# Optimization experiments

Measured on AMD Instinct MI355X. Metric: run time of the kernel, lower is better.

Reference implementation:

```python
import jax, jax.numpy as jnp
import numpy as np

H = 8
LN_EPS = 1e-5

def setup_inputs() -> dict:
    key = jax.random.key(0)
    k1, k2, k3, k4 = jax.random.split(key, 4)
    bh, q_len, dk = 64, 1024, 64
    return {
        "query": jax.random.normal(k1, (bh, q_len, dk), dtype=jnp.float32),
        "key": jax.random.normal(k2, (bh, q_len, dk), dtype=jnp.float32),
        "value": jax.random.normal(k3, (bh, q_len, dk), dtype=jnp.float32),
        "head_att": jax.random.normal(k4, (H, H), dtype=jnp.float32),
        "ln_w": jnp.ones((H,), dtype=jnp.float32),
        "ln_b": jnp.zeros((H,), dtype=jnp.float32),
    }

def reference(query, key, value, head_att, ln_w, ln_b):
    bh, q_len, dk = query.shape
    k_len = key.shape[1]
    # scores: (bh, q, k)
    scores = jnp.einsum("bqd,bkd->bqk", query, key) / jnp.sqrt(jnp.asarray(dk, query.dtype))
    attn = jax.nn.softmax(scores, axis=-1)
    # view as (B, H, q, k) then move heads last: (B, q, k, H)
    a = attn.reshape(-1, H, q_len, k_len).transpose(0, 2, 3, 1)
    # DeepViT re-attention: cross-head mixing matmul
    a = a @ head_att  # (B, q, k, H)
    # LayerNorm over head dim
    mu = a.mean(axis=-1, keepdims=True)
    var = ((a - mu) ** 2).mean(axis=-1, keepdims=True)
    a = (a - mu) * jax.lax.rsqrt(var + LN_EPS) * ln_w + ln_b
    # back to (B, H, q, k)
    a = a.transpose(0, 3, 1, 2)
    att_map = a.mean(axis=1)  # (B, q, k)
    attention = a.reshape(bh, q_len, k_len)
    out = jnp.einsum("bqk,bkd->bqd", attention, value)
    return (out, att_map)
```

## Files before the change

kernel.cpp:

```cpp
#include <hip/hip_runtime.h>
#include <hip/hip_bf16.h>

typedef _Float16 f16;
typedef f16 f16x8 __attribute__((ext_vector_type(8)));
typedef f16 f16x4 __attribute__((ext_vector_type(4)));
typedef float f32x4 __attribute__((ext_vector_type(4)));

#define QL 1024
#define KL 1024
#define DKD 64
#define NH 8
#define LNEPS 1e-5f

__global__ __launch_bounds__(256) void prep_cvt(const float* __restrict__ src,
                                                f16* __restrict__ dst, float scale) {
  int i = (blockIdx.x * 256 + threadIdx.x) * 4;
  float4 v = *reinterpret_cast<const float4*>(src + i);
  f16x4 o;
  o[0] = (f16)(v.x * scale); o[1] = (f16)(v.y * scale);
  o[2] = (f16)(v.z * scale); o[3] = (f16)(v.w * scale);
  *reinterpret_cast<f16x4*>(dst + i) = o;
}

__global__ __launch_bounds__(256) void prep_vt(const float* __restrict__ V, f16* __restrict__ vt) {
  __shared__ float t[32][33];
  const int bh = blockIdx.z, k0 = blockIdx.x * 32, d0 = blockIdx.y * 32;
  const float* src = V + ((size_t)bh * KL + k0) * DKD + d0;
#pragma unroll
  for (int j = 0; j < 4; ++j) {
    int kk = threadIdx.y * 4 + j;
    t[kk][threadIdx.x] = src[kk * DKD + threadIdx.x];
  }
  __syncthreads();
  f16* dst = vt + ((size_t)bh * DKD + d0) * KL + k0;
#pragma unroll
  for (int j = 0; j < 4; ++j) {
    int dd = threadIdx.y * 4 + j;
    dst[dd * KL + threadIdx.x] = (f16)t[threadIdx.x][dd];
  }
}

__global__ __launch_bounds__(256) void stats_kernel(const f16* __restrict__ qf,
    const f16* __restrict__ kf, float* __restrict__ rowsum) {
  const int tid = threadIdx.x;
  const int lane = tid & 63, w = tid >> 6;
  const int m = lane & 15, g = lane >> 4;
  const int id = blockIdx.x;
  const int bh = (id & 7) * 8 + ((id >> 3) & 7);
  const int q0 = (id >> 6) * 64 + w * 16;

  f16x8 qv[2];
#pragma unroll
  for (int dc = 0; dc < 2; ++dc)
    qv[dc] = *reinterpret_cast<const f16x8*>(
        qf + ((size_t)bh * QL + q0 + m) * DKD + dc * 32 + g * 8);

  float part[4] = {0.f, 0.f, 0.f, 0.f};
#pragma unroll 2
  for (int kt = 0; kt < 64; ++kt) {
    const f16* kb = kf + ((size_t)bh * KL + kt * 16 + m) * DKD + g * 8;
    f16x8 k0f = *reinterpret_cast<const f16x8*>(kb);
    f16x8 k1f = *reinterpret_cast<const f16x8*>(kb + 32);
    f32x4 acc = {0.f, 0.f, 0.f, 0.f};
    acc = __builtin_amdgcn_mfma_f32_16x16x32_f16(qv[0], k0f, acc, 0, 0, 0);
    acc = __builtin_amdgcn_mfma_f32_16x16x32_f16(qv[1], k1f, acc, 0, 0, 0);
#pragma unroll
    for (int ri = 0; ri < 4; ++ri) part[ri] += __expf(acc[ri]);
  }
#pragma unroll
  for (int ri = 0; ri < 4; ++ri) {
    float v = part[ri];
    v += __shfl_xor(v, 1); v += __shfl_xor(v, 2);
    v += __shfl_xor(v, 4); v += __shfl_xor(v, 8);
    part[ri] = v;
  }
  if (m == 0) {
#pragma unroll
    for (int ri = 0; ri < 4; ++ri) rowsum[(size_t)bh * QL + q0 + g * 4 + ri] = part[ri];
  }
}

__global__ __launch_bounds__(256) void main_kernel(
    const f16* __restrict__ qf, const f16* __restrict__ kf, const f16* __restrict__ vt,
    const float* __restrict__ rowsum,
    const float* __restrict__ hA, const float* __restrict__ lnw, const float* __restrict__ lnb,
    float* __restrict__ outp, float* __restrict__ part1, float* __restrict__ att_map) {
  __shared__ __align__(16) f16 y_lds[2][NH][16][64];

  const int tid = threadIdx.x;
  const int lane = tid & 63, w = tid >> 6;
  const int m = lane & 15, g = lane >> 4;
  const int id = blockIdx.x;
  const int b = id & 7, kc = (id >> 3) & 1, q0 = (id >> 4) * 16;

  float haR[64], wR[8], bR[8];
#pragma unroll
  for (int j = 0; j < 64; ++j) haR[j] = hA[j];
#pragma unroll
  for (int j = 0; j < 8; ++j) { wR[j] = lnw[j]; bR[j] = lnb[j]; }

  f16x8 qv[NH][2];
#pragma unroll
  for (int h = 0; h < NH; ++h)
#pragma unroll
    for (int dc = 0; dc < 2; ++dc)
      qv[h][dc] = *reinterpret_cast<const f16x8*>(
          qf + (((size_t)(b * NH + h)) * QL + q0 + m) * DKD + dc * 32 + g * 8);

  float inv_rs[NH][4];
#pragma unroll
  for (int h = 0; h < NH; ++h)
#pragma unroll
    for (int ri = 0; ri < 4; ++ri)
      inv_rs[h][ri] = 1.0f / rowsum[(size_t)(b * NH + h) * QL + q0 + g * 4 + ri];

  const size_t kbase_b = (size_t)b * NH * KL;
  f32x4 oacc[2][4];
#pragma unroll
  for (int hp = 0; hp < 2; ++hp)
#pragma unroll
    for (int dt = 0; dt < 4; ++dt) oacc[hp][dt] = (f32x4){0.f, 0.f, 0.f, 0.f};

  for (int kt = 0; kt < 8; ++kt) {
    const int kbase = kc * 512 + kt * 64;
    const int kcol = kbase + w * 16;
    const int buf = kt & 1;

    f32x4 pacc[NH];
    {
      const f16* kb = kf + (kbase_b + kcol + m) * DKD + g * 8;
#pragma unroll
      for (int h = 0; h < NH; ++h) {
        f16x8 k0f = *reinterpret_cast<const f16x8*>(kb + (size_t)h * KL * DKD);
        f16x8 k1f = *reinterpret_cast<const f16x8*>(kb + (size_t)h * KL * DKD + 32);
        f32x4 acc = {0.f, 0.f, 0.f, 0.f};
        acc = __builtin_amdgcn_mfma_f32_16x16x32_f16(qv[h][0], k0f, acc, 0, 0, 0);
        acc = __builtin_amdgcn_mfma_f32_16x16x32_f16(qv[h][1], k1f, acc, 0, 0, 0);
        pacc[h] = acc;
      }
    }
#pragma unroll
    for (int h = 0; h < NH; ++h)
#pragma unroll
      for (int ri = 0; ri < 4; ++ri)
        pacc[h][ri] = __expf(pacc[h][ri]) * inv_rs[h][ri];

#pragma unroll
    for (int ri = 0; ri < 4; ++ri) {
      const int qq = g * 4 + ri;
      float mixed[8];
      float mu = 0.f;
#pragma unroll
      for (int hh = 0; hh < 8; ++hh) {
        float s = 0.f;
#pragma unroll
        for (int j = 0; j < 8; ++j) s = fmaf(pacc[j][ri], haR[j * 8 + hh], s);
        mixed[hh] = s; mu += s;
      }
      mu *= 0.125f;
      float var = 0.f;
#pragma unroll
      for (int hh = 0; hh < 8; ++hh) { float d = mixed[hh] - mu; var = fmaf(d, d, var); }
      var *= 0.125f;
      const float rsv = rsqrtf(var + LNEPS);
      float am = 0.f;
      const int kidx = ((((2 * w + (m >> 3)) ^ (qq & 7)) << 3) | (m & 7));
#pragma unroll
      for (int hh = 0; hh < 8; ++hh) {
        float y = (mixed[hh] - mu) * rsv * wR[hh] + bR[hh];
        am += y;
        y_lds[buf][hh][qq][kidx] = (f16)y;
      }
      att_map[((size_t)b * QL + q0 + qq) * KL + kcol + m] = am * 0.125f;
    }
    __syncthreads();

#pragma unroll
    for (int hp = 0; hp < 2; ++hp) {
      const int hh = w + hp * 4;
      const f16* vb = vt + (((size_t)(b * NH + hh)) * DKD + m) * KL + kbase + g * 8;
#pragma unroll
      for (int ks = 0; ks < 2; ++ks) {
        const f16x8 af = *reinterpret_cast<const f16x8*>(
            &y_lds[buf][hh][m][((ks * 4 + g) ^ (m & 7)) << 3]);
#pragma unroll
        for (int dt = 0; dt < 4; ++dt) {
          f16x8 vf = *reinterpret_cast<const f16x8*>(vb + (size_t)dt * 16 * KL + ks * 32);
          oacc[hp][dt] = __builtin_amdgcn_mfma_f32_16x16x32_f16(af, vf, oacc[hp][dt], 0, 0, 0);
        }
      }
    }
  }

  float* dst = kc ? part1 : outp;
#pragma unroll
  for (int hp = 0; hp < 2; ++hp) {
    const int hh = w + hp * 4;
#pragma unroll
    for (int dt = 0; dt < 4; ++dt)
#pragma unroll
      for (int ri = 0; ri < 4; ++ri)
        dst[(((size_t)(b * NH + hh)) * QL + q0 + g * 4 + ri) * DKD + dt * 16 + m] =
            oacc[hp][dt][ri];
  }
}

__global__ __launch_bounds__(256) void reduce_kernel(const float* __restrict__ p1,
                                                     float* __restrict__ outp) {
  size_t i = ((size_t)blockIdx.x * 256 + threadIdx.x) * 4;
  float4 a = *reinterpret_cast<const float4*>(outp + i);
  float4 c = *reinterpret_cast<const float4*>(p1 + i);
  a.x += c.x; a.y += c.y; a.z += c.z; a.w += c.w;
  *reinterpret_cast<float4*>(outp + i) = a;
}

extern "C" void kernel_launch(void* const* d_in, const int* in_sizes, int n_in,
                              void* d_out, int out_size, void* d_ws, size_t ws_size,
                              hipStream_t stream) {
  const float* Qm  = (const float*)d_in[0];
  const float* Km  = (const float*)d_in[1];
  const float* Vm  = (const float*)d_in[2];
  const float* hA  = (const float*)d_in[3];
  const float* lnw = (const float*)d_in[4];
  const float* lnb = (const float*)d_in[5];
  float* outp = (float*)d_out;
  float* att_map = outp + (size_t)64 * QL * DKD;

  char* ws = (char*)d_ws;
  f16* kfp   = (f16*)ws;
  f16* vtp   = (f16*)(ws + (size_t)8388608);
  f16* qfp   = (f16*)(ws + (size_t)16777216);
  float* rsm = (float*)(ws + (size_t)25165824);
  float* p1  = (float*)(ws + (size_t)25427968);

  prep_cvt<<<4096, 256, 0, stream>>>(Km, kfp, 1.0f);
  prep_cvt<<<4096, 256, 0, stream>>>(Qm, qfp, 0.125f);
  prep_vt<<<dim3(32, 2, 64), dim3(32, 8), 0, stream>>>(Vm, vtp);
  stats_kernel<<<1024, 256, 0, stream>>>(qfp, kfp, rsm);
  main_kernel<<<1024, 256, 0, stream>>>(qfp, kfp, vtp, rsm, hA, lnw, lnb, outp, p1, att_map);
  reduce_kernel<<<4096, 256, 0, stream>>>(p1, outp);
}
```

Baseline: 240.8 us.

## Split fused attention into mix and PV kernels with packed fp16 head mixing

```diff
diff --git a/kernel.cpp b/kernel.cpp
--- a/kernel.cpp
+++ b/kernel.cpp
@@ -1,10 +1,12 @@
 #include <hip/hip_runtime.h>
-#include <hip/hip_bf16.h>
 
 typedef _Float16 f16;
 typedef f16 f16x8 __attribute__((ext_vector_type(8)));
 typedef f16 f16x4 __attribute__((ext_vector_type(4)));
+typedef f16 hf2 __attribute__((ext_vector_type(2)));
 typedef float f32x4 __attribute__((ext_vector_type(4)));
+typedef unsigned int u32;
+typedef unsigned short u16;
 
 #define QL 1024
 #define KL 1024
@@ -12,9 +14,27 @@
 #define NH 8
 #define LNEPS 1e-5f
 
-__global__ __launch_bounds__(256) void prep_cvt(const float* __restrict__ src,
-                                                f16* __restrict__ dst, float scale) {
-  int i = (blockIdx.x * 256 + threadIdx.x) * 4;
+__device__ __forceinline__ hf2 pkrtz(float a, float b) {
+  return __builtin_bit_cast(hf2, __builtin_amdgcn_cvt_pkrtz(a, b));
+}
+__device__ __forceinline__ hf2 bch(u32 v) { return __builtin_bit_cast(hf2, v); }
+
+__global__ __launch_bounds__(256) void prep_qk(const float* __restrict__ K,
+    const float* __restrict__ Q, f16* __restrict__ kf, f16* __restrict__ qf,
+    const float* __restrict__ hA, const float* __restrict__ lnw,
+    const float* __restrict__ lnb, u32* __restrict__ prm) {
+  const int bid = blockIdx.x;
+  if (bid == 0 && threadIdx.x < 80) {
+    int t = threadIdx.x;
+    float v = t < 64 ? hA[t] : (t < 72 ? lnw[t - 64] : lnb[t - 72]);
+    u16 hb = __builtin_bit_cast(u16, (f16)v);
+    prm[t] = (u32)hb * 0x10001u;
+  }
+  const bool isQ = bid >= 4096;
+  const float* src = isQ ? Q : K;
+  f16* dst = isQ ? qf : kf;
+  const float scale = isQ ? 0.125f : 1.0f;
+  int i = ((bid & 4095) * 256 + threadIdx.x) * 4;
   float4 v = *reinterpret_cast<const float4*>(src + i);
   f16x4 o;
   o[0] = (f16)(v.x * scale); o[1] = (f16)(v.y * scale);
@@ -40,30 +60,30 @@
   }
 }
 
-__global__ __launch_bounds__(256) void stats_kernel(const f16* __restrict__ qf,
-    const f16* __restrict__ kf, float* __restrict__ rowsum) {
-  const int tid = threadIdx.x;
-  const int lane = tid & 63, w = tid >> 6;
+__global__ __launch_bounds__(256) void stats4(const f16* __restrict__ qf,
+    const f16* __restrict__ kf, float* __restrict__ prs4) {
+  const int tid = threadIdx.x, lane = tid & 63, w = tid >> 6;
   const int m = lane & 15, g = lane >> 4;
-  const int id = blockIdx.x;
-  const int bh = (id & 7) * 8 + ((id >> 3) & 7);
-  const int q0 = (id >> 6) * 64 + w * 16;
-
-  f16x8 qv[2];
-#pragma unroll
-  for (int dc = 0; dc < 2; ++dc)
-    qv[dc] = *reinterpret_cast<const f16x8*>(
-        qf + ((size_t)bh * QL + q0 + m) * DKD + dc * 32 + g * 8);
+  int id = blockIdx.x;
+  const int b = id & 7; id >>= 3;
+  const int h = id & 7; id >>= 3;
+  const int kq = id & 3; const int q64 = id >> 2;
+  const int bh = b * 8 + h;
+  const int q0 = q64 * 64 + w * 16;
+
+  const f16* qp = qf + ((size_t)bh * QL + q0 + m) * DKD + g * 8;
+  f16x8 qv0 = *reinterpret_cast<const f16x8*>(qp);
+  f16x8 qv1 = *reinterpret_cast<const f16x8*>(qp + 32);
 
   float part[4] = {0.f, 0.f, 0.f, 0.f};
 #pragma unroll 2
-  for (int kt = 0; kt < 64; ++kt) {
-    const f16* kb = kf + ((size_t)bh * KL + kt * 16 + m) * DKD + g * 8;
+  for (int kt = 0; kt < 16; ++kt) {
+    const f16* kb = kf + ((size_t)bh * KL + kq * 256 + kt * 16 + m) * DKD + g * 8;
     f16x8 k0f = *reinterpret_cast<const f16x8*>(kb);
     f16x8 k1f = *reinterpret_cast<const f16x8*>(kb + 32);
     f32x4 acc = {0.f, 0.f, 0.f, 0.f};
-    acc = __builtin_amdgcn_mfma_f32_16x16x32_f16(qv[0], k0f, acc, 0, 0, 0);
-    acc = __builtin_amdgcn_mfma_f32_16x16x32_f16(qv[1], k1f, acc, 0, 0, 0);
+    acc = __builtin_amdgcn_mfma_f32_16x16x32_f16(qv0, k0f, acc, 0, 0, 0);
+    acc = __builtin_amdgcn_mfma_f32_16x16x32_f16(qv1, k1f, acc, 0, 0, 0);
 #pragma unroll
     for (int ri = 0; ri < 4; ++ri) part[ri] += __expf(acc[ri]);
   }
@@ -76,142 +96,146 @@
   }
   if (m == 0) {
 #pragma unroll
-    for (int ri = 0; ri < 4; ++ri) rowsum[(size_t)bh * QL + q0 + g * 4 + ri] = part[ri];
-  }
-}
-
-__global__ __launch_bounds__(256) void main_kernel(
-    const f16* __restrict__ qf, const f16* __restrict__ kf, const f16* __restrict__ vt,
-    const float* __restrict__ rowsum,
-    const float* __restrict__ hA, const float* __restrict__ lnw, const float* __restrict__ lnb,
-    float* __restrict__ outp, float* __restrict__ part1, float* __restrict__ att_map) {
-  __shared__ __align__(16) f16 y_lds[2][NH][16][64];
-
-  const int tid = threadIdx.x;
-  const int lane = tid & 63, w = tid >> 6;
+    for (int ri = 0; ri < 4; ++ri)
+      prs4[((size_t)kq * 64 + bh) * QL + q0 + g * 4 + ri] = part[ri];
+  }
+}
+
+__global__ __launch_bounds__(256) void stats_red(const float* __restrict__ prs4,
+                                                 float* __restrict__ lrs) {
+  int i = (blockIdx.x * 256 + threadIdx.x) * 4;
+  float4 a = *reinterpret_cast<const float4*>(prs4 + i);
+  float4 c = *reinterpret_cast<const float4*>(prs4 + 65536 + i);
+  float4 d = *reinterpret_cast<const float4*>(prs4 + 131072 + i);
+  float4 e = *reinterpret_cast<const float4*>(prs4 + 196608 + i);
+  float4 o;
+  o.x = __logf(a.x + c.x + d.x + e.x);
+  o.y = __logf(a.y + c.y + d.y + e.y);
+  o.z = __logf(a.z + c.z + d.z + e.z);
+  o.w = __logf(a.w + c.w + d.w + e.w);
+  *reinterpret_cast<float4*>(lrs + i) = o;
+}
+
+__global__ __launch_bounds__(256) void mix_kernel(const f16* __restrict__ qf,
+    const f16* __restrict__ kf, const float* __restrict__ lrs_g,
+    const u32* __restrict__ prm, f16* __restrict__ yq, float* __restrict__ att_map,
+    int qs) {
+  const int tid = threadIdx.x, lane = tid & 63, w = tid >> 6;
   const int m = lane & 15, g = lane >> 4;
-  const int id = blockIdx.x;
-  const int b = id & 7, kc = (id >> 3) & 1, q0 = (id >> 4) * 16;
-
-  float haR[64], wR[8], bR[8];
-#pragma unroll
-  for (int j = 0; j < 64; ++j) haR[j] = hA[j];
-#pragma unroll
-  for (int j = 0; j < 8; ++j) { wR[j] = lnw[j]; bR[j] = lnb[j]; }
-
-  f16x8 qv[NH][2];
-#pragma unroll
-  for (int h = 0; h < NH; ++h)
-#pragma unroll
-    for (int dc = 0; dc < 2; ++dc)
-      qv[h][dc] = *reinterpret_cast<const f16x8*>(
-          qf + (((size_t)(b * NH + h)) * QL + q0 + m) * DKD + dc * 32 + g * 8);
-
-  float inv_rs[NH][4];
-#pragma unroll
-  for (int h = 0; h < NH; ++h)
-#pragma unroll
-    for (int ri = 0; ri < 4; ++ri)
-      inv_rs[h][ri] = 1.0f / rowsum[(size_t)(b * NH + h) * QL + q0 + g * 4 + ri];
-
-  const size_t kbase_b = (size_t)b * NH * KL;
-  f32x4 oacc[2][4];
-#pragma unroll
-  for (int hp = 0; hp < 2; ++hp)
-#pragma unroll
-    for (int dt = 0; dt < 4; ++dt) oacc[hp][dt] = (f32x4){0.f, 0.f, 0.f, 0.f};
-
-  for (int kt = 0; kt < 8; ++kt) {
-    const int kbase = kc * 512 + kt * 64;
-    const int kcol = kbase + w * 16;
-    const int buf = kt & 1;
-
-    f32x4 pacc[NH];
-    {
-      const f16* kb = kf + (kbase_b + kcol + m) * DKD + g * 8;
-#pragma unroll
-      for (int h = 0; h < NH; ++h) {
-        f16x8 k0f = *reinterpret_cast<const f16x8*>(kb + (size_t)h * KL * DKD);
-        f16x8 k1f = *reinterpret_cast<const f16x8*>(kb + (size_t)h * KL * DKD + 32);
-        f32x4 acc = {0.f, 0.f, 0.f, 0.f};
-        acc = __builtin_amdgcn_mfma_f32_16x16x32_f16(qv[h][0], k0f, acc, 0, 0, 0);
-        acc = __builtin_amdgcn_mfma_f32_16x16x32_f16(qv[h][1], k1f, acc, 0, 0, 0);
-        pacc[h] = acc;
+  int id = blockIdx.x;
+  const int b = id & 7; id >>= 3;
+  const int k32 = id & 31; const int q64t = id >> 5;
+  const int q0 = qs * 256 + q64t * 64 + w * 16;
+  const int qrow = q0 + g * 4;
+  const int qLrow = q64t * 64 + w * 16 + g * 4;
+
+  u32 prmL[80];
+#pragma unroll
+  for (int j = 0; j < 80; ++j) prmL[j] = prm[j];
+
+  float lrs[NH][4];
+#pragma unroll
+  for (int h = 0; h < NH; ++h) {
+    f32x4 l4 = *reinterpret_cast<const f32x4*>(lrs_g + (((size_t)(b * 8 + h)) << 10) + qrow);
+#pragma unroll
+    for (int ri = 0; ri < 4; ++ri) lrs[h][ri] = l4[ri];
+  }
+
+  const hf2 c125 = {(f16)0.125f, (f16)0.125f};
+
+  for (int kt = 0; kt < 2; ++kt) {
+    const int k0 = k32 * 32 + kt * 16;
+    hf2 pP[NH][2];
+#pragma unroll
+    for (int h = 0; h < NH; ++h) {
+      const f16* qp = qf + ((((size_t)(b * 8 + h)) << 10) + q0 + m) * DKD + g * 8;
+      const f16* kp = kf + ((((size_t)(b * 8 + h)) << 10) + k0 + m) * DKD + g * 8;
+      f32x4 acc = {0.f, 0.f, 0.f, 0.f};
+      acc = __builtin_amdgcn_mfma_f32_16x16x32_f16(
+          *reinterpret_cast<const f16x8*>(qp), *reinterpret_cast<const f16x8*>(kp), acc, 0, 0, 0);
+      acc = __builtin_amdgcn_mfma_f32_16x16x32_f16(
+          *reinterpret_cast<const f16x8*>(qp + 32), *reinterpret_cast<const f16x8*>(kp + 32), acc, 0, 0, 0);
+      pP[h][0] = pkrtz(__expf(acc[0] - lrs[h][0]), __expf(acc[1] - lrs[h][1]));
+      pP[h][1] = pkrtz(__expf(acc[2] - lrs[h][2]), __expf(acc[3] - lrs[h][3]));
+    }
+    hf2 mx[NH][2];
+#pragma unroll
+    for (int hh = 0; hh < NH; ++hh)
+#pragma unroll
+      for (int pp = 0; pp < 2; ++pp) {
+        hf2 acc = pP[0][pp] * bch(prmL[hh]);
+#pragma unroll
+        for (int j = 1; j < 8; ++j) acc += pP[j][pp] * bch(prmL[j * 8 + hh]);
+        mx[hh][pp] = acc;
       }
-    }
-#pragma unroll
-    for (int h = 0; h < NH; ++h)
-#pragma unroll
-      for (int ri = 0; ri < 4; ++ri)
-        pacc[h][ri] = __expf(pacc[h][ri]) * inv_rs[h][ri];
-
-#pragma unroll
-    for (int ri = 0; ri < 4; ++ri) {
-      const int qq = g * 4 + ri;
-      float mixed[8];
-      float mu = 0.f;
-#pragma unroll
-      for (int hh = 0; hh < 8; ++hh) {
-        float s = 0.f;
-#pragma unroll
-        for (int j = 0; j < 8; ++j) s = fmaf(pacc[j][ri], haR[j * 8 + hh], s);
-        mixed[hh] = s; mu += s;
+    hf2 mu[2], var[2];
+#pragma unroll
+    for (int pp = 0; pp < 2; ++pp) {
+      hf2 s = mx[0][pp];
+#pragma unroll
+      for (int hh = 1; hh < NH; ++hh) s += mx[hh][pp];
+      mu[pp] = s * c125;
+    }
+#pragma unroll
+    for (int pp = 0; pp < 2; ++pp) {
+      hf2 v = {};
+#pragma unroll
+      for (int hh = 0; hh < NH; ++hh) {
+        mx[hh][pp] -= mu[pp];
+        v += mx[hh][pp] * mx[hh][pp];
       }
-      mu *= 0.125f;
-      float var = 0.f;
-#pragma unroll
-      for (int hh = 0; hh < 8; ++hh) { float d = mixed[hh] - mu; var = fmaf(d, d, var); }
-      var *= 0.125f;
-      const float rsv = rsqrtf(var + LNEPS);
-      float am = 0.f;
-      const int kidx = ((((2 * w + (m >> 3)) ^ (qq & 7)) << 3) | (m & 7));
-#pragma unroll
-      for (int hh = 0; hh < 8; ++hh) {
-        float y = (mixed[hh] - mu) * rsv * wR[hh] + bR[hh];
-        am += y;
-        y_lds[buf][hh][qq][kidx] = (f16)y;
+      var[pp] = v * c125;
+    }
+    float r0 = rsqrtf((float)var[0][0] + LNEPS);
+    float r1 = rsqrtf((float)var[0][1] + LNEPS);
+    float r2 = rsqrtf((float)var[1][0] + LNEPS);
+    float r3 = rsqrtf((float)var[1][1] + LNEPS);
+    hf2 rsv[2] = {pkrtz(r0, r1), pkrtz(r2, r3)};
+    hf2 am[2] = {{}, {}};
+#pragma unroll
+    for (int hh = 0; hh < NH; ++hh) {
+      f16* yb = yq + ((((size_t)(b * 8 + hh)) << 8) + qLrow) * KL + k0 + m;
+#pragma unroll
+      for (int pp = 0; pp < 2; ++pp) {
+        hf2 t = mx[hh][pp] * rsv[pp];
+        hf2 y = t * bch(prmL[64 + hh]) + bch(prmL[72 + hh]);
+        am[pp] += y;
+        yb[(2 * pp) * KL] = y[0];
+        yb[(2 * pp + 1) * KL] = y[1];
       }
-      att_map[((size_t)b * QL + q0 + qq) * KL + kcol + m] = am * 0.125f;
-    }
-    __syncthreads();
-
-#pragma unroll
-    for (int hp = 0; hp < 2; ++hp) {
-      const int hh = w + hp * 4;
-      const f16* vb = vt + (((size_t)(b * NH + hh)) * DKD + m) * KL + kbase + g * 8;
-#pragma unroll
-      for (int ks = 0; ks < 2; ++ks) {
-        const f16x8 af = *reinterpret_cast<const f16x8*>(
-            &y_lds[buf][hh][m][((ks * 4 + g) ^ (m & 7)) << 3]);
-#pragma unroll
-        for (int dt = 0; dt < 4; ++dt) {
-          f16x8 vf = *reinterpret_cast<const f16x8*>(vb + (size_t)dt * 16 * KL + ks * 32);
-          oacc[hp][dt] = __builtin_amdgcn_mfma_f32_16x16x32_f16(af, vf, oacc[hp][dt], 0, 0, 0);
-        }
-      }
-    }
-  }
-
-  float* dst = kc ? part1 : outp;
-#pragma unroll
-  for (int hp = 0; hp < 2; ++hp) {
-    const int hh = w + hp * 4;
-#pragma unroll
-    for (int dt = 0; dt < 4; ++dt)
-#pragma unroll
-      for (int ri = 0; ri < 4; ++ri)
-        dst[(((size_t)(b * NH + hh)) * QL + q0 + g * 4 + ri) * DKD + dt * 16 + m] =
-            oacc[hp][dt][ri];
-  }
-}
-
-__global__ __launch_bounds__(256) void reduce_kernel(const float* __restrict__ p1,
-                                                     float* __restrict__ outp) {
-  size_t i = ((size_t)blockIdx.x * 256 + threadIdx.x) * 4;
-  float4 a = *reinterpret_cast<const float4*>(outp + i);
-  float4 c = *reinterpret_cast<const float4*>(p1 + i);
-  a.x += c.x; a.y += c.y; a.z += c.z; a.w += c.w;
-  *reinterpret_cast<float4*>(outp + i) = a;
+    }
+    float* ab = att_map + ((((size_t)b) << 10) + qrow) * KL + k0 + m;
+    ab[0]        = (float)am[0][0] * 0.125f;
+    ab[KL]       = (float)am[0][1] * 0.125f;
+    ab[2 * KL]   = (float)am[1][0] * 0.125f;
+    ab[3 * KL]   = (float)am[1][1] * 0.125f;
+  }
+}
+
+__global__ __launch_bounds__(256) void pv_kernel(const f16* __restrict__ yq,
+    const f16* __restrict__ vt, float* __restrict__ outp, int qs) {
+  const int tid = threadIdx.x, lane = tid & 63, w = tid >> 6;
+  const int m = lane & 15, g = lane >> 4;
+  int id = blockIdx.x;
+  const int b = id & 7; id >>= 3;
+  const int h = id & 7; id >>= 3;
+  const int q64t = id & 3; const int dq = id >> 2;
+  const int q0L = q64t * 64 + w * 16;
+  const int bh = b * 8 + h;
+
+  const f16* ab = yq + ((((size_t)bh) << 8) + q0L + m) * KL + g * 8;
+  const f16* bb = vt + ((size_t)bh * DKD + dq * 16 + m) * KL + g * 8;
+  f32x4 acc = {0.f, 0.f, 0.f, 0.f};
+#pragma unroll 4
+  for (int kk = 0; kk < 32; ++kk) {
+    f16x8 af = *reinterpret_cast<const f16x8*>(ab + kk * 32);
+    f16x8 bf = *reinterpret_cast<const f16x8*>(bb + kk * 32);
+    acc = __builtin_amdgcn_mfma_f32_16x16x32_f16(af, bf, acc, 0, 0, 0);
+  }
+  const int q = qs * 256 + q0L + g * 4;
+  float* ob = outp + ((((size_t)bh) << 10) + q) * DKD + dq * 16 + m;
+#pragma unroll
+  for (int ri = 0; ri < 4; ++ri) ob[ri * DKD] = acc[ri];
 }
 
 extern "C" void kernel_launch(void* const* d_in, const int* in_sizes, int n_in,
@@ -227,16 +251,20 @@
   float* att_map = outp + (size_t)64 * QL * DKD;
 
   char* ws = (char*)d_ws;
-  f16* kfp   = (f16*)ws;
-  f16* vtp   = (f16*)(ws + (size_t)8388608);
-  f16* qfp   = (f16*)(ws + (size_t)16777216);
-  float* rsm = (float*)(ws + (size_t)25165824);
-  float* p1  = (float*)(ws + (size_t)25427968);
-
-  prep_cvt<<<4096, 256, 0, stream>>>(Km, kfp, 1.0f);
-  prep_cvt<<<4096, 256, 0, stream>>>(Qm, qfp, 0.125f);
+  f16* kfp    = (f16*)ws;
+  f16* vtp    = (f16*)(ws + (size_t)8388608);
+  f16* qfp    = (f16*)(ws + (size_t)16777216);
+  float* prs4 = (float*)(ws + (size_t)25165824);
+  float* lrs  = (float*)(ws + (size_t)26214400);
+  u32* prm    = (u32*)(ws + (size_t)27262976);
+  f16* yqb    = (f16*)(ws + (size_t)28311552);
+
+  prep_qk<<<8192, 256, 0, stream>>>(Km, Qm, kfp, qfp, hA, lnw, lnb, prm);
   prep_vt<<<dim3(32, 2, 64), dim3(32, 8), 0, stream>>>(Vm, vtp);
-  stats_kernel<<<1024, 256, 0, stream>>>(qfp, kfp, rsm);
-  main_kernel<<<1024, 256, 0, stream>>>(qfp, kfp, vtp, rsm, hA, lnw, lnb, outp, p1, att_map);
-  reduce_kernel<<<4096, 256, 0, stream>>>(p1, outp);
-}
+  stats4<<<4096, 256, 0, stream>>>(qfp, kfp, prs4);
+  stats_red<<<256, 256, 0, stream>>>(prs4, lrs);
+  for (int qs = 0; qs < 4; ++qs) {
+    mix_kernel<<<1024, 256, 0, stream>>>(qfp, kfp, lrs, prm, yqb, att_map, qs);
+    pv_kernel<<<1024, 256, 0, stream>>>(yqb, vtp, outp, qs);
+  }
+}
```

Result: slower. 345.7 us (+43.6%).
